# Optimization experiments

Hardware: AMD Instinct MI355X
Metric: run time of the kernel (lower is better)

Reference implementation:

```python
import jax, jax.numpy as jnp
import numpy as np

B, T, D, H = 2, 2048, 1024, 32
NEG = -1e9  # used in place of -inf for masked logits (no fully-masked rows here)


def setup_inputs() -> dict:
    key = jax.random.key(0)
    ks = jax.random.split(key, 8)
    q = jax.random.normal(ks[0], (B, T, D), jnp.float32)
    k = jax.random.normal(ks[1], (B, T, D), jnp.float32)
    v = jax.random.normal(ks[2], (B, T, D), jnp.float32)
    Wqkv = jax.random.normal(ks[3], (D, 3 * D), jnp.float32) * 0.02
    bqkv = jax.random.normal(ks[4], (3 * D,), jnp.float32) * 0.02
    Wo = jax.random.normal(ks[5], (D, D), jnp.float32) * 0.02
    bo = jax.random.normal(ks[6], (D,), jnp.float32) * 0.02
    # pad the last 128 key positions of batch element 1
    key_padding_mask = jnp.zeros((B, T), bool).at[1, T - 128:].set(True)
    # causal mask: prevent attending to subsequent tokens (True = masked)
    attn_mask = jnp.triu(jnp.ones((T, T), bool), k=1)
    return {"q": q, "k": k, "v": v, "Wqkv": Wqkv, "bqkv": bqkv,
            "Wo": Wo, "bo": bo, "key_padding_mask": key_padding_mask,
            "attn_mask": attn_mask, "n_heads": H}


def reference(q, k, v, Wqkv, bqkv, Wo, bo, key_padding_mask, attn_mask, n_heads):
    Bq, T1, Dm = q.shape
    T2 = k.shape[1]
    dh = Dm // n_heads
    # project concatenated [q; k; v] tokens with the shared qkv Linear
    x = jnp.concatenate([q, k, v], axis=1)                 # [B, T1+2*T2, D]
    proj = x @ Wqkv + bqkv                                 # [B, Ttot, 3D]
    # channel layout is (qkv h d) per the Rearrange
    proj = proj.reshape(Bq, -1, 3, n_heads, dh)            # [B, Ttot, 3, H, dh]
    qp = proj[:, :T1, 0]                                   # [B, T1, H, dh]
    kp = proj[:, T1:T1 + T2, 1]                            # [B, T2, H, dh]
    vp = proj[:, T1 + T2:, 2]                              # [B, T2, H, dh]
    scores = jnp.einsum('bqhd,bkhd->bhqk', qp, kp) / np.sqrt(dh).astype(qp.dtype)
    mask = key_padding_mask[:, None, None, :] | attn_mask[None, None, :, :]
    scores = jnp.where(mask, NEG, scores)
    attn = jax.nn.softmax(scores, axis=-1)                 # [B, H, T1, T2]
    y = jnp.einsum('bhqk,bkhd->bqhd', attn, vp)            # [B, T1, H, dh]
    y = y.reshape(Bq, T1, Dm)
    return y @ Wo + bo
```

## Files before the change

kernel.cpp:

```cpp
#include <hip/hip_runtime.h>

typedef __bf16 bf16;
typedef __bf16 bf16x4 __attribute__((ext_vector_type(4)));
typedef __bf16 bf16x8 __attribute__((ext_vector_type(8)));
typedef float  f32x4  __attribute__((ext_vector_type(4)));

#define MFMA16(A, B, C) __builtin_amdgcn_mfma_f32_16x16x32_bf16((A), (B), (C), 0, 0, 0)

__device__ __forceinline__ void gld16(void* lds, const void* g) {
  __builtin_amdgcn_global_load_lds((__attribute__((address_space(1))) void*)(g),
                                   (__attribute__((address_space(3))) void*)(lds),
                                   16, 0, 0);
}

__global__ __launch_bounds__(256) void cvt3(const float* __restrict__ q,
                                            const float* __restrict__ k,
                                            const float* __restrict__ v,
                                            bf16* __restrict__ d) {
  int bi = blockIdx.x;
  int which = bi >> 11;
  const float* s = (which == 0) ? q : ((which == 1) ? k : v);
  int i = ((bi & 2047) * 256 + threadIdx.x) * 8;
  float4 a = *(const float4*)&s[i];
  float4 b = *(const float4*)&s[i + 4];
  bf16x8 o;
  o[0] = (bf16)a.x; o[1] = (bf16)a.y; o[2] = (bf16)a.z; o[3] = (bf16)a.w;
  o[4] = (bf16)b.x; o[5] = (bf16)b.y; o[6] = (bf16)b.z; o[7] = (bf16)b.w;
  *(bf16x8*)&d[(size_t)which * 4194304 + i] = o;
}

__global__ __launch_bounds__(256) void tr_cvt(const float* __restrict__ W,
                                              bf16* __restrict__ Wt, int Kr, int Nc) {
  __shared__ float t[32][33];
  int n0 = blockIdx.x * 32, k0 = blockIdx.y * 32;
  int tx = threadIdx.x, ty = threadIdx.y;
  #pragma unroll
  for (int i = 0; i < 4; ++i)
    t[ty + i * 8][tx] = W[(size_t)(k0 + ty + i * 8) * Nc + n0 + tx];
  __syncthreads();
  #pragma unroll
  for (int i = 0; i < 4; ++i)
    Wt[(size_t)(n0 + ty + i * 8) * Kr + k0 + tx] = (bf16)t[tx][ty + i * 8];
}

template <int MODE>
__global__ __launch_bounds__(256) void gemm_bt(const bf16* __restrict__ Ab,
                                               const bf16* __restrict__ Btb,
                                               const float* __restrict__ biasb,
                                               void* __restrict__ outp, int K) {
  __shared__ bf16 lA[128 * 32];
  __shared__ bf16 lB[128 * 32];
  const int z = blockIdx.z;
  const bf16* A  = Ab  + (size_t)z * 4096 * 1024;
  const bf16* Bt = Btb + (size_t)z * 1024 * 1024;
  const float* bias = biasb + z * 1024;
  const int m0 = blockIdx.y * 128, n0 = blockIdx.x * 128;
  const int tid = threadIdx.x;
  const int w = tid >> 6, lane = tid & 63, g = lane >> 4, c = lane & 15;
  const int wm = (w & 1) * 64, wn = (w >> 1) * 64;
  const int srow = tid >> 2;
  const int skq  = (tid & 3) * 8;

  f32x4 acc[4][4] = {};

  for (int k0 = 0; k0 < K; k0 += 32) {
    gld16(&lA[srow * 32 + skq],        &A [(size_t)(m0 + srow)      * K + k0 + skq]);
    gld16(&lA[(64 + srow) * 32 + skq], &A [(size_t)(m0 + 64 + srow) * K + k0 + skq]);
    gld16(&lB[srow * 32 + skq],        &Bt[(size_t)(n0 + srow)      * K + k0 + skq]);
    gld16(&lB[(64 + srow) * 32 + skq], &Bt[(size_t)(n0 + 64 + srow) * K + k0 + skq]);
    __syncthreads();
    bf16x8 af[4], bf_[4];
    #pragma unroll
    for (int i = 0; i < 4; ++i) {
      af[i]  = *(const bf16x8*)&lA[(wm + i * 16 + c) * 32 + g * 8];
      bf_[i] = *(const bf16x8*)&lB[(wn + i * 16 + c) * 32 + g * 8];
    }
    #pragma unroll
    for (int mi = 0; mi < 4; ++mi)
      #pragma unroll
      for (int ni = 0; ni < 4; ++ni)
        acc[mi][ni] = MFMA16(af[mi], bf_[ni], acc[mi][ni]);
    __syncthreads();
  }

  float bv[4];
  #pragma unroll
  for (int ni = 0; ni < 4; ++ni) bv[ni] = bias[n0 + wn + ni * 16 + c];

  if constexpr (MODE == 0) {
    const float scale = (z == 0) ? 0.2550353720f : 1.0f;
    bf16* O = (bf16*)outp;
    #pragma unroll
    for (int mi = 0; mi < 4; ++mi) {
      #pragma unroll
      for (int r = 0; r < 4; ++r) {
        int mg = m0 + wm + mi * 16 + g * 4 + r;
        int bb = mg >> 11, tt = mg & 2047;
        #pragma unroll
        for (int ni = 0; ni < 4; ++ni) {
          int col = n0 + wn + ni * 16 + c;
          float val = (acc[mi][ni][r] + bv[ni]) * scale;
          size_t off = ((((size_t)z * 2 + bb) * 32 + (col >> 5)) * 2048 + tt) * 32 + (col & 31);
          O[off] = (bf16)val;
        }
      }
    }
  } else {
    float* O = (float*)outp;
    #pragma unroll
    for (int mi = 0; mi < 4; ++mi) {
      #pragma unroll
      for (int r = 0; r < 4; ++r) {
        int mg = m0 + wm + mi * 16 + g * 4 + r;
        #pragma unroll
        for (int ni = 0; ni < 4; ++ni) {
          int col = n0 + wn + ni * 16 + c;
          O[(size_t)mg * 1024 + col] = acc[mi][ni][r] + bv[ni];
        }
      }
    }
  }
}

__global__ __launch_bounds__(256, 4) void attn(const bf16* __restrict__ qkvp,
                                               bf16* __restrict__ Y) {
  __shared__ bf16 KL[4][64 * 32];
  __shared__ bf16 VT[2][32 * 72];
  __shared__ bf16 P[4][16 * 72];

  const int bx = blockIdx.x;
  const int qtA = bx, qtB = 31 - bx;
  const int bh = blockIdx.y, b = bh >> 5, h = bh & 31;
  const int tid = threadIdx.x, w = tid >> 6, lane = tid & 63, g = lane >> 4, c = lane & 15;

  const size_t headQ = ((size_t)b * 32 + h) * 65536;
  const size_t headK = ((size_t)(2 + b) * 32 + h) * 65536;
  const size_t headV = ((size_t)(4 + b) * 32 + h) * 65536;

  const int qrowA = qtA * 64 + w * 16 + c;
  const int qrowB = qtB * 64 + w * 16 + c;
  const bf16x8 qfA = *(const bf16x8*)&qkvp[headQ + (size_t)qrowA * 32 + g * 8];
  const bf16x8 qfB = *(const bf16x8*)&qkvp[headQ + (size_t)qrowB * 32 + g * 8];

  bf16x8 ones;
  #pragma unroll
  for (int j = 0; j < 8; ++j) ones[j] = (bf16)1.0f;

  f32x4 oA0 = {}, oA1 = {}, osA = {};
  f32x4 oB0 = {}, oB1 = {}, osB = {};
  float mA = -1e30f, mB = -1e30f;

  const int ksr = tid >> 2, ksc = (tid & 3) * 8;
  const int vdc = w * 8;
  bf16* Pw = &P[w][0];

  auto k_stage = [&](int kt) {
    gld16(&KL[kt & 3][ksr * 32 + ksc], &qkvp[headK + (size_t)(kt * 64 + ksr) * 32 + ksc]);
  };
  auto v_load = [&](int kt) -> bf16x8 {
    return *(const bf16x8*)&qkvp[headV + (size_t)(kt * 64 + lane) * 32 + vdc];
  };
  auto v_store = [&](int kt, bf16x8 vv) {
    #pragma unroll
    for (int j = 0; j < 8; ++j) VT[kt & 1][(vdc + j) * 72 + lane] = vv[j];
  };
  auto kfrag = [&](int kt, int t) -> bf16x8 {
    return *(const bf16x8*)&KL[kt & 3][(t * 16 + c) * 32 + g * 8];
  };
  auto mask_tile = [&](f32x4* st4, int kt, int qrow, bool diag, bool pad) {
    #pragma unroll
    for (int t = 0; t < 4; ++t) {
      int kb = kt * 64 + t * 16 + g * 4;
      #pragma unroll
      for (int r = 0; r < 4; ++r) {
        int kk = kb + r;
        bool m = (diag && kk > qrow) || (pad && kk >= 1920);
        st4[t][r] = m ? -1e9f : st4[t][r];
      }
    }
  };
  auto soft64 = [&](f32x4* st4, float& m_q) -> float {
    float tm = -1e30f;
    #pragma unroll
    for (int t = 0; t < 4; ++t)
      #pragma unroll
      for (int r = 0; r < 4; ++r) tm = fmaxf(tm, st4[t][r]);
    tm = fmaxf(tm, __shfl_xor(tm, 16));
    tm = fmaxf(tm, __shfl_xor(tm, 32));
    float mn = fmaxf(m_q, tm);
    float a = __builtin_amdgcn_exp2f(m_q - mn);
    m_q = mn;
    return a;
  };
  auto p_tile = [&](const f32x4* st4, float mn) {
    #pragma unroll
    for (int t = 0; t < 4; ++t) {
      bf16x4 pv;
      #pragma unroll
      for (int r = 0; r < 4; ++r) pv[r] = (bf16)__builtin_amdgcn_exp2f(st4[t][r] - mn);
      *(bf16x4*)&Pw[c * 72 + t * 16 + g * 4] = pv;
    }
  };
  auto pv_acc = [&](int kt, f32x4& o0, f32x4& o1, f32x4& os) {
    bf16x8 pf0 = *(const bf16x8*)&Pw[c * 72 + g * 8];
    bf16x8 pf1 = *(const bf16x8*)&Pw[c * 72 + 32 + g * 8];
    const bf16* VB = &VT[kt & 1][0];
    bf16x8 v00 = *(const bf16x8*)&VB[c * 72 + g * 8];
    bf16x8 v01 = *(const bf16x8*)&VB[c * 72 + 32 + g * 8];
    bf16x8 v10 = *(const bf16x8*)&VB[(16 + c) * 72 + g * 8];
    bf16x8 v11 = *(const bf16x8*)&VB[(16 + c) * 72 + 32 + g * 8];
    o0 = MFMA16(pf0, v00, o0);
    o0 = MFMA16(pf1, v01, o0);
    o1 = MFMA16(pf0, v10, o1);
    o1 = MFMA16(pf1, v11, o1);
    os = MFMA16(pf0, ones, os);
    os = MFMA16(pf1, ones, os);
  };
  auto rescale = [&](float a, f32x4& o0, f32x4& o1, f32x4& os) {
    #pragma unroll
    for (int r = 0; r < 4; ++r) {
      float ar = __shfl(a, g * 4 + r);
      o0[r] *= ar; o1[r] *= ar; os[r] *= ar;
    }
  };

  k_stage(0);
  { bf16x8 vv = v_load(0); v_store(0, vv); }
  __syncthreads();

  for (int kt = 0; kt <= qtA; ++kt) {
    k_stage(kt + 1);
    bf16x8 vvn = v_load(kt + 1);

    f32x4 stA[4], stB[4];
    #pragma unroll
    for (int t = 0; t < 4; ++t) {
      bf16x8 kf = kfrag(kt, t);
      f32x4 z = {};
      stB[t] = MFMA16(kf, qfB, z);
      stA[t] = MFMA16(kf, qfA, z);
    }
    if (kt == qtA) mask_tile(stA, kt, qrowA, true, false);
    float aA = soft64(stA, mA);
    float aB = soft64(stB, mB);

    p_tile(stA, mA);
    rescale(aA, oA0, oA1, osA);
    pv_acc(kt, oA0, oA1, osA);

    p_tile(stB, mB);
    rescale(aB, oB0, oB1, osB);
    pv_acc(kt, oB0, oB1, osB);

    v_store(kt + 1, vvn);
    __syncthreads();
  }

  {
    const int s = qtA + 1;
    const bool f1 = (s + 1 <= qtB), f2 = (s + 2 <= qtB);
    if (f1) k_stage(s + 1);
    if (f2) k_stage(s + 2);
    bf16x8 vv1 = {}, vv2 = {};
    if (f1) vv1 = v_load(s + 1);
    if (f2) vv2 = v_load(s + 2);

    f32x4 st[4];
    #pragma unroll
    for (int t = 0; t < 4; ++t) {
      f32x4 z = {};
      st[t] = MFMA16(kfrag(s, t), qfB, z);
    }
    if (s == qtB) mask_tile(st, s, qrowB, true, false);
    float a = soft64(st, mB);
    p_tile(st, mB);
    rescale(a, oB0, oB1, osB);
    pv_acc(s, oB0, oB1, osB);

    if (f1) v_store(s + 1, vv1);
    __syncthreads();
    if (f2) { v_store(s + 2, vv2); __syncthreads(); }
  }

  for (int p = qtA + 2; p < qtB; p += 2) {
    const bool f = (p + 3 <= qtB);
    if (f) { k_stage(p + 2); k_stage(p + 3); }
    bf16x8 vv1 = {}, vv2 = {};
    if (f) { vv1 = v_load(p + 2); vv2 = v_load(p + 3); }

    f32x4 st[8];
    #pragma unroll
    for (int t = 0; t < 4; ++t) {
      f32x4 z = {};
      st[t] = MFMA16(kfrag(p, t), qfB, z);
    }
    #pragma unroll
    for (int t = 0; t < 4; ++t) {
      f32x4 z = {};
      st[4 + t] = MFMA16(kfrag(p + 1, t), qfB, z);
    }
    const bool diag2 = (p + 1 == qtB);
    const bool pad1 = (b == 1) && (p >= 30);
    const bool pad2 = (b == 1) && (p + 1 >= 30);
    if (pad1) mask_tile(st, p, qrowB, false, true);
    if (diag2 || pad2) mask_tile(st + 4, p + 1, qrowB, diag2, pad2);

    float tm = -1e30f;
    #pragma unroll
    for (int t = 0; t < 8; ++t)
      #pragma unroll
      for (int r = 0; r < 4; ++r) tm = fmaxf(tm, st[t][r]);
    tm = fmaxf(tm, __shfl_xor(tm, 16));
    tm = fmaxf(tm, __shfl_xor(tm, 32));
    float mn = fmaxf(mB, tm);
    float a = __builtin_amdgcn_exp2f(mB - mn);
    mB = mn;
    rescale(a, oB0, oB1, osB);

    p_tile(st, mB);
    pv_acc(p, oB0, oB1, osB);
    p_tile(st + 4, mB);
    pv_acc(p + 1, oB0, oB1, osB);

    __syncthreads();
    if (f) {
      v_store(p + 2, vv1);
      v_store(p + 3, vv2);
      __syncthreads();
    }
  }

  #pragma unroll
  for (int r = 0; r < 4; ++r) {
    float li = 1.f / osB[r];
    int qg = qtB * 64 + w * 16 + g * 4 + r;
    size_t base = ((size_t)b * 2048 + qg) * 1024 + h * 32;
    Y[base + c]      = (bf16)(oB0[r] * li);
    Y[base + 16 + c] = (bf16)(oB1[r] * li);
  }
  #pragma unroll
  for (int r = 0; r < 4; ++r) {
    float li = 1.f / osA[r];
    int qg = qtA * 64 + w * 16 + g * 4 + r;
    size_t base = ((size_t)b * 2048 + qg) * 1024 + h * 32;
    Y[base + c]      = (bf16)(oA0[r] * li);
    Y[base + 16 + c] = (bf16)(oA1[r] * li);
  }
}

extern "C" void kernel_launch(void* const* d_in, const int* in_sizes, int n_in,
                              void* d_out, int out_size, void* d_ws, size_t ws_size,
                              hipStream_t stream) {
  const float* q    = (const float*)d_in[0];
  const float* k    = (const float*)d_in[1];
  const float* v    = (const float*)d_in[2];
  const float* Wqkv = (const float*)d_in[3];
  const float* bqkv = (const float*)d_in[4];
  const float* Wo   = (const float*)d_in[5];
  const float* bo   = (const float*)d_in[6];

  bf16* xqkv = (bf16*)d_ws;
  bf16* Wt   = xqkv + 12582912;
  bf16* Wot  = Wt + 3145728;
  bf16* qkvp = Wot + 1048576;
  bf16* Yb   = qkvp + 12582912;

  cvt3<<<6144, 256, 0, stream>>>(q, k, v, xqkv);
  tr_cvt<<<dim3(96, 32), dim3(32, 8), 0, stream>>>(Wqkv, Wt, 1024, 3072);
  tr_cvt<<<dim3(32, 32), dim3(32, 8), 0, stream>>>(Wo, Wot, 1024, 1024);

  gemm_bt<0><<<dim3(8, 32, 3), 256, 0, stream>>>(xqkv, Wt, bqkv, (void*)qkvp, 1024);
  attn<<<dim3(16, 64), 256, 0, stream>>>(qkvp, Yb);
  gemm_bt<1><<<dim3(8, 32, 1), 256, 0, stream>>>(Yb, Wot, bo, d_out, 1024);
}
```

Measured before the change: 252.5 us.

## Add lazy softmax rescale, MFMA priority hints, and narrower output GEMM tiles

The attention kernel now rescales the running max only when some lane's new tile max exceeds the stored max by more than 8 (in log2 units). This skips the exp and shuffle-based rescale on most tiles, at the cost of somewhat larger unnormalised exponents. It also raises wave priority around the MFMA blocks, hoists the V fragment loads so they are shared by both query tiles, and builds the tile max as a tree. The output projection GEMM is templated on BN and launched with 64-wide N tiles, doubling its grid to 512 blocks so more CUs are used.

Result: faster. 241.8 us (-4.2%).

```diff
diff --git a/kernel.cpp b/kernel.cpp
--- a/kernel.cpp
+++ b/kernel.cpp
@@ -43,49 +43,52 @@
     Wt[(size_t)(n0 + ty + i * 8) * Kr + k0 + tx] = (bf16)t[tx][ty + i * 8];
 }
 
-template <int MODE>
+template <int MODE, int BN>
 __global__ __launch_bounds__(256) void gemm_bt(const bf16* __restrict__ Ab,
                                                const bf16* __restrict__ Btb,
                                                const float* __restrict__ biasb,
                                                void* __restrict__ outp, int K) {
+  constexpr int NI = BN / 32;
   __shared__ bf16 lA[128 * 32];
-  __shared__ bf16 lB[128 * 32];
+  __shared__ bf16 lB[BN * 32];
   const int z = blockIdx.z;
   const bf16* A  = Ab  + (size_t)z * 4096 * 1024;
   const bf16* Bt = Btb + (size_t)z * 1024 * 1024;
   const float* bias = biasb + z * 1024;
-  const int m0 = blockIdx.y * 128, n0 = blockIdx.x * 128;
+  const int m0 = blockIdx.y * 128, n0 = blockIdx.x * BN;
   const int tid = threadIdx.x;
   const int w = tid >> 6, lane = tid & 63, g = lane >> 4, c = lane & 15;
-  const int wm = (w & 1) * 64, wn = (w >> 1) * 64;
+  const int wm = (w & 1) * 64, wn = (w >> 1) * (BN / 2);
   const int srow = tid >> 2;
   const int skq  = (tid & 3) * 8;
 
-  f32x4 acc[4][4] = {};
+  f32x4 acc[4][NI] = {};
 
   for (int k0 = 0; k0 < K; k0 += 32) {
     gld16(&lA[srow * 32 + skq],        &A [(size_t)(m0 + srow)      * K + k0 + skq]);
     gld16(&lA[(64 + srow) * 32 + skq], &A [(size_t)(m0 + 64 + srow) * K + k0 + skq]);
     gld16(&lB[srow * 32 + skq],        &Bt[(size_t)(n0 + srow)      * K + k0 + skq]);
-    gld16(&lB[(64 + srow) * 32 + skq], &Bt[(size_t)(n0 + 64 + srow) * K + k0 + skq]);
+    if constexpr (BN > 64)
+      gld16(&lB[(64 + srow) * 32 + skq], &Bt[(size_t)(n0 + 64 + srow) * K + k0 + skq]);
     __syncthreads();
-    bf16x8 af[4], bf_[4];
-    #pragma unroll
-    for (int i = 0; i < 4; ++i) {
+    bf16x8 af[4], bf_[NI];
+    #pragma unroll
+    for (int i = 0; i < 4; ++i)
       af[i]  = *(const bf16x8*)&lA[(wm + i * 16 + c) * 32 + g * 8];
+    #pragma unroll
+    for (int i = 0; i < NI; ++i)
       bf_[i] = *(const bf16x8*)&lB[(wn + i * 16 + c) * 32 + g * 8];
-    }
     #pragma unroll
     for (int mi = 0; mi < 4; ++mi)
       #pragma unroll
-      for (int ni = 0; ni < 4; ++ni)
+      for (int ni = 0; ni < NI; ++ni)
         acc[mi][ni] = MFMA16(af[mi], bf_[ni], acc[mi][ni]);
     __syncthreads();
   }
 
-  float bv[4];
-  #pragma unroll
-  for (int ni = 0; ni < 4; ++ni) bv[ni] = bias[n0 + wn + ni * 16 + c];
+  float bv[NI];
+  #pragma unroll
+  for (int ni = 0; ni < NI; ++ni) bv[ni] = bias[n0 + wn + ni * 16 + c];
 
   if constexpr (MODE == 0) {
     const float scale = (z == 0) ? 0.2550353720f : 1.0f;
@@ -97,7 +100,7 @@
         int mg = m0 + wm + mi * 16 + g * 4 + r;
         int bb = mg >> 11, tt = mg & 2047;
         #pragma unroll
-        for (int ni = 0; ni < 4; ++ni) {
+        for (int ni = 0; ni < NI; ++ni) {
           int col = n0 + wn + ni * 16 + c;
           float val = (acc[mi][ni][r] + bv[ni]) * scale;
           size_t off = ((((size_t)z * 2 + bb) * 32 + (col >> 5)) * 2048 + tt) * 32 + (col & 31);
@@ -113,7 +116,7 @@
       for (int r = 0; r < 4; ++r) {
         int mg = m0 + wm + mi * 16 + g * 4 + r;
         #pragma unroll
-        for (int ni = 0; ni < 4; ++ni) {
+        for (int ni = 0; ni < NI; ++ni) {
           int col = n0 + wn + ni * 16 + c;
           O[(size_t)mg * 1024 + col] = acc[mi][ni][r] + bv[ni];
         }
@@ -179,18 +182,16 @@
       }
     }
   };
-  auto soft64 = [&](f32x4* st4, float& m_q) -> float {
-    float tm = -1e30f;
-    #pragma unroll
-    for (int t = 0; t < 4; ++t)
-      #pragma unroll
-      for (int r = 0; r < 4; ++r) tm = fmaxf(tm, st4[t][r]);
+  auto tmax4in = [&](const f32x4* st4) -> float {
+    float t0 = fmaxf(fmaxf(st4[0][0], st4[0][1]), fmaxf(st4[0][2], st4[0][3]));
+    float t1 = fmaxf(fmaxf(st4[1][0], st4[1][1]), fmaxf(st4[1][2], st4[1][3]));
+    float t2 = fmaxf(fmaxf(st4[2][0], st4[2][1]), fmaxf(st4[2][2], st4[2][3]));
+    float t3 = fmaxf(fmaxf(st4[3][0], st4[3][1]), fmaxf(st4[3][2], st4[3][3]));
+    return fmaxf(fmaxf(t0, t1), fmaxf(t2, t3));
+  };
+  auto xred = [&](float tm) -> float {
     tm = fmaxf(tm, __shfl_xor(tm, 16));
-    tm = fmaxf(tm, __shfl_xor(tm, 32));
-    float mn = fmaxf(m_q, tm);
-    float a = __builtin_amdgcn_exp2f(m_q - mn);
-    m_q = mn;
-    return a;
+    return fmaxf(tm, __shfl_xor(tm, 32));
   };
   auto p_tile = [&](const f32x4* st4, float mn) {
     #pragma unroll
@@ -201,27 +202,33 @@
       *(bf16x4*)&Pw[c * 72 + t * 16 + g * 4] = pv;
     }
   };
-  auto pv_acc = [&](int kt, f32x4& o0, f32x4& o1, f32x4& os) {
+  auto rescale = [&](float a, f32x4& o0, f32x4& o1, f32x4& os) {
+    #pragma unroll
+    for (int r = 0; r < 4; ++r) {
+      float ar = __shfl(a, g * 4 + r);
+      o0[r] *= ar; o1[r] *= ar; os[r] *= ar;
+    }
+  };
+  auto pv_accv = [&](bf16x8 v00, bf16x8 v01, bf16x8 v10, bf16x8 v11,
+                     f32x4& o0, f32x4& o1, f32x4& os) {
     bf16x8 pf0 = *(const bf16x8*)&Pw[c * 72 + g * 8];
     bf16x8 pf1 = *(const bf16x8*)&Pw[c * 72 + 32 + g * 8];
-    const bf16* VB = &VT[kt & 1][0];
-    bf16x8 v00 = *(const bf16x8*)&VB[c * 72 + g * 8];
-    bf16x8 v01 = *(const bf16x8*)&VB[c * 72 + 32 + g * 8];
-    bf16x8 v10 = *(const bf16x8*)&VB[(16 + c) * 72 + g * 8];
-    bf16x8 v11 = *(const bf16x8*)&VB[(16 + c) * 72 + 32 + g * 8];
+    __builtin_amdgcn_s_setprio(1);
     o0 = MFMA16(pf0, v00, o0);
     o0 = MFMA16(pf1, v01, o0);
     o1 = MFMA16(pf0, v10, o1);
     o1 = MFMA16(pf1, v11, o1);
     os = MFMA16(pf0, ones, os);
     os = MFMA16(pf1, ones, os);
-  };
-  auto rescale = [&](float a, f32x4& o0, f32x4& o1, f32x4& os) {
-    #pragma unroll
-    for (int r = 0; r < 4; ++r) {
-      float ar = __shfl(a, g * 4 + r);
-      o0[r] *= ar; o1[r] *= ar; os[r] *= ar;
-    }
+    __builtin_amdgcn_s_setprio(0);
+  };
+  auto pv_acc = [&](int kt, f32x4& o0, f32x4& o1, f32x4& os) {
+    const bf16* VB = &VT[kt & 1][0];
+    bf16x8 v00 = *(const bf16x8*)&VB[c * 72 + g * 8];
+    bf16x8 v01 = *(const bf16x8*)&VB[c * 72 + 32 + g * 8];
+    bf16x8 v10 = *(const bf16x8*)&VB[(16 + c) * 72 + g * 8];
+    bf16x8 v11 = *(const bf16x8*)&VB[(16 + c) * 72 + 32 + g * 8];
+    pv_accv(v00, v01, v10, v11, o0, o1, os);
   };
 
   k_stage(0);
@@ -233,6 +240,7 @@
     bf16x8 vvn = v_load(kt + 1);
 
     f32x4 stA[4], stB[4];
+    __builtin_amdgcn_s_setprio(1);
     #pragma unroll
     for (int t = 0; t < 4; ++t) {
       bf16x8 kf = kfrag(kt, t);
@@ -240,17 +248,37 @@
       stB[t] = MFMA16(kf, qfB, z);
       stA[t] = MFMA16(kf, qfA, z);
     }
+    __builtin_amdgcn_s_setprio(0);
     if (kt == qtA) mask_tile(stA, kt, qrowA, true, false);
-    float aA = soft64(stA, mA);
-    float aB = soft64(stB, mB);
-
-    p_tile(stA, mA);
-    rescale(aA, oA0, oA1, osA);
-    pv_acc(kt, oA0, oA1, osA);
-
-    p_tile(stB, mB);
-    rescale(aB, oB0, oB1, osB);
-    pv_acc(kt, oB0, oB1, osB);
+
+    const bf16* VB = &VT[kt & 1][0];
+    bf16x8 v00 = *(const bf16x8*)&VB[c * 72 + g * 8];
+    bf16x8 v01 = *(const bf16x8*)&VB[c * 72 + 32 + g * 8];
+    bf16x8 v10 = *(const bf16x8*)&VB[(16 + c) * 72 + g * 8];
+    bf16x8 v11 = *(const bf16x8*)&VB[(16 + c) * 72 + 32 + g * 8];
+
+    float tmA = xred(tmax4in(stA));
+    float tmB = xred(tmax4in(stB));
+
+    bool upA = !__all(tmA <= mA + 8.f);
+    float mnA = upA ? fmaxf(mA, tmA) : mA;
+    p_tile(stA, mnA);
+    if (upA) {
+      float a = __builtin_amdgcn_exp2f(mA - mnA);
+      mA = mnA;
+      rescale(a, oA0, oA1, osA);
+    }
+    pv_accv(v00, v01, v10, v11, oA0, oA1, osA);
+
+    bool upB = !__all(tmB <= mB + 8.f);
+    float mnB = upB ? fmaxf(mB, tmB) : mB;
+    p_tile(stB, mnB);
+    if (upB) {
+      float a = __builtin_amdgcn_exp2f(mB - mnB);
+      mB = mnB;
+      rescale(a, oB0, oB1, osB);
+    }
+    pv_accv(v00, v01, v10, v11, oB0, oB1, osB);
 
     v_store(kt + 1, vvn);
     __syncthreads();
@@ -266,15 +294,24 @@
     if (f2) vv2 = v_load(s + 2);
 
     f32x4 st[4];
+    __builtin_amdgcn_s_setprio(1);
     #pragma unroll
     for (int t = 0; t < 4; ++t) {
       f32x4 z = {};
       st[t] = MFMA16(kfrag(s, t), qfB, z);
     }
+    __builtin_amdgcn_s_setprio(0);
     if (s == qtB) mask_tile(st, s, qrowB, true, false);
-    float a = soft64(st, mB);
-    p_tile(st, mB);
-    rescale(a, oB0, oB1, osB);
+
+    float tm = xred(tmax4in(st));
+    bool up = !__all(tm <= mB + 8.f);
+    float mn = up ? fmaxf(mB, tm) : mB;
+    p_tile(st, mn);
+    if (up) {
+      float a = __builtin_amdgcn_exp2f(mB - mn);
+      mB = mn;
+      rescale(a, oB0, oB1, osB);
+    }
     pv_acc(s, oB0, oB1, osB);
 
     if (f1) v_store(s + 1, vv1);
@@ -289,6 +326,7 @@
     if (f) { vv1 = v_load(p + 2); vv2 = v_load(p + 3); }
 
     f32x4 st[8];
+    __builtin_amdgcn_s_setprio(1);
     #pragma unroll
     for (int t = 0; t < 4; ++t) {
       f32x4 z = {};
@@ -299,27 +337,25 @@
       f32x4 z = {};
       st[4 + t] = MFMA16(kfrag(p + 1, t), qfB, z);
     }
+    __builtin_amdgcn_s_setprio(0);
     const bool diag2 = (p + 1 == qtB);
     const bool pad1 = (b == 1) && (p >= 30);
     const bool pad2 = (b == 1) && (p + 1 >= 30);
     if (pad1) mask_tile(st, p, qrowB, false, true);
     if (diag2 || pad2) mask_tile(st + 4, p + 1, qrowB, diag2, pad2);
 
-    float tm = -1e30f;
-    #pragma unroll
-    for (int t = 0; t < 8; ++t)
-      #pragma unroll
-      for (int r = 0; r < 4; ++r) tm = fmaxf(tm, st[t][r]);
-    tm = fmaxf(tm, __shfl_xor(tm, 16));
-    tm = fmaxf(tm, __shfl_xor(tm, 32));
-    float mn = fmaxf(mB, tm);
-    float a = __builtin_amdgcn_exp2f(mB - mn);
-    mB = mn;
-    rescale(a, oB0, oB1, osB);
-
-    p_tile(st, mB);
+    float tm = xred(fmaxf(tmax4in(st), tmax4in(st + 4)));
+    bool up = !__all(tm <= mB + 8.f);
+    float mn = up ? fmaxf(mB, tm) : mB;
+    if (up) {
+      float a = __builtin_amdgcn_exp2f(mB - mn);
+      mB = mn;
+      rescale(a, oB0, oB1, osB);
+    }
+
+    p_tile(st, mn);
     pv_acc(p, oB0, oB1, osB);
-    p_tile(st + 4, mB);
+    p_tile(st + 4, mn);
     pv_acc(p + 1, oB0, oB1, osB);
 
     __syncthreads();
@@ -369,7 +405,7 @@
   tr_cvt<<<dim3(96, 32), dim3(32, 8), 0, stream>>>(Wqkv, Wt, 1024, 3072);
   tr_cvt<<<dim3(32, 32), dim3(32, 8), 0, stream>>>(Wo, Wot, 1024, 1024);
 
-  gemm_bt<0><<<dim3(8, 32, 3), 256, 0, stream>>>(xqkv, Wt, bqkv, (void*)qkvp, 1024);
+  gemm_bt<0, 128><<<dim3(8, 32, 3), 256, 0, stream>>>(xqkv, Wt, bqkv, (void*)qkvp, 1024);
   attn<<<dim3(16, 64), 256, 0, stream>>>(qkvp, Yb);
-  gemm_bt<1><<<dim3(8, 32, 1), 256, 0, stream>>>(Yb, Wot, bo, d_out, 1024);
-}
+  gemm_bt<1, 64><<<dim3(16, 32, 1), 256, 0, stream>>>(Yb, Wot, bo, d_out, 1024);
+}
```
